# Optimization experiments

Hardware: AMD Instinct MI355X
Metric: run time of the kernel (lower is better)

The kernel has to match this reference:

```python
import jax, jax.numpy as jnp
import numpy as np

QLEN, B, D = 1024, 4, 512
H, DH = 8, 64
MEM, DMLP = 1024, 2048
KLEN = MEM + QLEN
EPS = 1e-5


def layer_norm(x, g, b):
    mu = jnp.mean(x, axis=-1, keepdims=True)
    var = jnp.var(x, axis=-1, keepdims=True)
    return (x - mu) * jax.lax.rsqrt(var + EPS) * g + b


def rel_shift(x):
    # x: [qlen, klen, b, h] -- Transformer-XL relative shift trick
    q, k, b, h = x.shape
    zp = jnp.zeros((q, 1, b, h), dtype=x.dtype)
    x = jnp.concatenate([zp, x], axis=1)          # [q, k+1, b, h]
    x = x.reshape(k + 1, q, b, h)[1:]             # drop first row
    return x.reshape(q, k, b, h)


def setup_inputs() -> dict:
    key = jax.random.key(0)
    ks = jax.random.split(key, 12)
    s = 0.02
    inp = {
        "inputs": jax.random.normal(ks[0], (QLEN, B, D), jnp.float32),
        "r": jax.random.normal(ks[1], (KLEN, D), jnp.float32),
        "u": jax.random.normal(ks[2], (H, DH), jnp.float32) * s,
        "v": jax.random.normal(ks[3], (H, DH), jnp.float32) * s,
        "mem": jax.random.normal(ks[4], (MEM, B, D), jnp.float32),
        # causal mask: query i (global pos MEM+i) cannot attend key j > MEM+i
        "attn_mask": jnp.arange(KLEN)[None, :] > (jnp.arange(QLEN)[:, None] + MEM),
        "Wqkv": jax.random.normal(ks[5], (3 * D, D), jnp.float32) * s,
        "Wr": jax.random.normal(ks[6], (D, D), jnp.float32) * s,
        "Wo": jax.random.normal(ks[7], (D, D), jnp.float32) * s,
        "ln1_g": jnp.ones((D,), jnp.float32),
        "ln1_b": jnp.zeros((D,), jnp.float32),
        "mlp_w1": jax.random.normal(ks[8], (DMLP, D), jnp.float32) * s,
        "mlp_b1": jnp.zeros((DMLP,), jnp.float32),
        "mlp_w2": jax.random.normal(ks[9], (D, DMLP), jnp.float32) * s,
        "mlp_b2": jnp.zeros((D,), jnp.float32),
        "ln2_g": jnp.ones((D,), jnp.float32),
        "ln2_b": jnp.zeros((D,), jnp.float32),
    }
    return inp


def reference(inputs, r, u, v, mem, attn_mask, Wqkv, Wr, Wo,
              ln1_g, ln1_b, mlp_w1, mlp_b1, mlp_w2, mlp_b2, ln2_g, ln2_b):
    qlen, b, d = inputs.shape
    cat = jnp.concatenate([mem, inputs], axis=0)          # [klen, b, d]
    klen = cat.shape[0]
    qkv = cat @ Wqkv.T                                    # [klen, b, 3d]
    q, k, w_v = jnp.split(qkv, 3, axis=-1)
    q = q[-qlen:].reshape(qlen, b, H, DH)
    k = k.reshape(klen, b, H, DH)
    w_v = w_v.reshape(klen, b, H, DH)
    rk = (r @ Wr.T).reshape(klen, H, DH)                  # [klen, h, dh]

    AC = jnp.einsum('ibhd,jbhd->ijbh', q + u, k)          # content term
    BD = jnp.einsum('ibhd,jhd->ijbh', q + v, rk)          # position term
    BD = rel_shift(BD)
    scale = 1.0 / np.sqrt(DH)
    score = (AC + BD) * scale                             # [q, k, b, h]
    score = jnp.where(attn_mask[:, :, None, None], jnp.float32(-1e30), score)
    prob = jax.nn.softmax(score, axis=1)
    attn = jnp.einsum('ijbh,jbhd->ibhd', prob, w_v).reshape(qlen, b, d)
    attn_out = attn @ Wo.T

    y = layer_norm(inputs + attn_out, ln1_g, ln1_b)
    h = jax.nn.relu(y @ mlp_w1.T + mlp_b1)
    z = h @ mlp_w2.T + mlp_b2
    out = layer_norm(y + z, ln2_g, ln2_b)
    return out, prob
```

## Files before the change

### kernel.cpp

```cpp
#include <hip/hip_runtime.h>
#include <math.h>

#define QL 1024
#define BSZ 4
#define DM 512
#define NH 8
#define DHH 64
#define MEML 1024
#define KL 2048
#define DMLP 2048

typedef __attribute__((ext_vector_type(8))) short bf16x8;
typedef __attribute__((ext_vector_type(4))) float f32x4;

#define MFMA16(A, B, C) __builtin_amdgcn_mfma_f32_16x16x32_bf16((A), (B), (C), 0, 0, 0)
#define SWZB(r, cb) (((r) << 7) + ((cb) ^ (((r) & 7) << 4)))
#define RINGB(r, c) (((r) << 9) + ((((c) << 2)) ^ (((r) & 7) << 4)))
#define CVT2(dst, lo, hi) \
  asm("v_cvt_pk_bf16_f32 %0, %1, %2" : "=v"(dst) : "v"(lo), "v"(hi))
#define GLOAD_LDS(gp, lp) __builtin_amdgcn_global_load_lds( \
    (const __attribute__((address_space(1))) void*)(gp), \
    (__attribute__((address_space(3))) void*)(lp), 16, 0, 0)

__device__ __forceinline__ void split_bf16(const float4 a, uint2& h, uint2& l) {
  CVT2(h.x, a.x, a.y); CVT2(h.y, a.z, a.w);
  float4 r;
  r.x = a.x - __uint_as_float(h.x << 16);
  r.y = a.y - __uint_as_float(h.x & 0xffff0000u);
  r.z = a.z - __uint_as_float(h.y << 16);
  r.w = a.w - __uint_as_float(h.y & 0xffff0000u);
  CVT2(l.x, r.x, r.y); CVT2(l.y, r.z, r.w);
}

__device__ __forceinline__ void store_tiled(char* hiB, char* loB, int KT,
                                            int row, int c0, uint2 h, uint2 l) {
  const size_t off = (((size_t)(row >> 7) * KT + (c0 >> 6)) << 14)
                   + SWZB(row & 127, (c0 & 63) * 2);
  *(uint2*)(hiB + off) = h;
  *(uint2*)(loB + off) = l;
}

__global__ __launch_bounds__(256)
void precvt_all(const float* __restrict__ mem, const float* __restrict__ inputs,
                const float* __restrict__ r, const float* __restrict__ Wqkv,
                const float* __restrict__ Wr, const float* __restrict__ Wo,
                const float* __restrict__ w1, const float* __restrict__ w2,
                unsigned short* CAThi, unsigned short* CATlo,
                unsigned short* Rhi, unsigned short* Rlo,
                unsigned short* Qhi, unsigned short* Qlo,
                unsigned short* WrHi, unsigned short* WrLo,
                unsigned short* WoHi, unsigned short* WoLo,
                unsigned short* w1Hi, unsigned short* w1Lo,
                unsigned short* w2Hi, unsigned short* w2Lo) {
  const int id = blockIdx.x * 256 + threadIdx.x;
  float4 a; uint2 h, l;
  if (id < 1048576) {
    const int row = id >> 7, c0 = (id & 127) * 4;
    const float* s = (row < 4096) ? mem + (size_t)row * 512
                                  : inputs + (size_t)(row - 4096) * 512;
    a = *(const float4*)(s + c0);
    split_bf16(a, h, l);
    store_tiled((char*)CAThi, (char*)CATlo, 8, row, c0, h, l);
  } else if (id < 1310720) {
    const int e = id - 1048576, row = e >> 7, c0 = (e & 127) * 4;
    a = *(const float4*)(r + (size_t)row * 512 + c0);
    split_bf16(a, h, l);
    store_tiled((char*)Rhi, (char*)Rlo, 8, row, c0, h, l);
  } else if (id < 1507328) {
    const int e = id - 1310720, row = e >> 7, c0 = (e & 127) * 4;
    a = *(const float4*)(Wqkv + (size_t)row * 512 + c0);
    split_bf16(a, h, l);
    store_tiled((char*)Qhi, (char*)Qlo, 8, row, c0, h, l);
  } else if (id < 1572864) {
    const int e = id - 1507328, row = e >> 7, c0 = (e & 127) * 4;
    a = *(const float4*)(Wr + (size_t)row * 512 + c0);
    split_bf16(a, h, l);
    store_tiled((char*)WrHi, (char*)WrLo, 8, row, c0, h, l);
  } else if (id < 1638400) {
    const int e = id - 1572864, row = e >> 7, c0 = (e & 127) * 4;
    a = *(const float4*)(Wo + (size_t)row * 512 + c0);
    split_bf16(a, h, l);
    store_tiled((char*)WoHi, (char*)WoLo, 8, row, c0, h, l);
  } else if (id < 1900544) {
    const int e = id - 1638400, row = e >> 7, c0 = (e & 127) * 4;
    a = *(const float4*)(w1 + (size_t)row * 512 + c0);
    split_bf16(a, h, l);
    store_tiled((char*)w1Hi, (char*)w1Lo, 8, row, c0, h, l);
  } else if (id < 2162688) {
    const int e = id - 1900544, row = e >> 9, c0 = (e & 511) * 4;
    a = *(const float4*)(w2 + (size_t)row * 2048 + c0);
    split_bf16(a, h, l);
    store_tiled((char*)w2Hi, (char*)w2Lo, 32, row, c0, h, l);
  }
}

__global__ __launch_bounds__(256)
void pack_kvr(const float* __restrict__ QKV, const float* __restrict__ RK,
              unsigned short* __restrict__ Kb, unsigned short* __restrict__ Rb,
              unsigned short* __restrict__ Vtb) {
  const int id = blockIdx.x * 256 + threadIdx.x;
  if (id < 1048576) {
    const int c4 = (id & 15) * 4;
    const int j  = (id >> 4) & 2047;
    const int bhv = id >> 15;
    const int bq = bhv >> 3, hq = bhv & 7;
    const float4 a = *(const float4*)(QKV + ((size_t)j * 4 + bq) * 1536 + 512 + hq * 64 + c4);
    uint2 p; CVT2(p.x, a.x, a.y); CVT2(p.y, a.z, a.w);
    *(uint2*)((char*)Kb + (((size_t)bhv * 32 + (j >> 6)) << 13) + SWZB(j & 63, c4 * 2)) = p;
  } else if (id < 1310720) {
    const int e = id - 1048576;
    const int c4 = (e & 15) * 4;
    const int jr = (e >> 4) & 2047;
    const int hq = e >> 15;
    const float4 a = *(const float4*)(RK + (size_t)jr * 512 + hq * 64 + c4);
    uint2 p; CVT2(p.x, a.x, a.y); CVT2(p.y, a.z, a.w);
    *(uint2*)((char*)Rb + (((size_t)hq * 32 + (jr >> 6)) << 13) + SWZB(jr & 63, c4 * 2)) = p;
  } else if (id < 1572864) {
    const int e = id - 1310720;
    const int d4 = (e & 15) * 4;
    const int jb = ((e >> 4) & 15) * 4;
    const int jt = (e >> 8) & 31;
    const int bhv = e >> 13;
    const int bq = bhv >> 3, hq = bhv & 7;
    const float* src = QKV + ((size_t)(jt * 64 + jb) * 4 + bq) * 1536 + 1024 + hq * 64 + d4;
    const float4 a0 = *(const float4*)(src);
    const float4 a1 = *(const float4*)(src + 6144);
    const float4 a2 = *(const float4*)(src + 12288);
    const float4 a3 = *(const float4*)(src + 18432);
    char* base = (char*)Vtb + (((size_t)bhv * 32 + jt) << 13);
    uint2 p;
    CVT2(p.x, a0.x, a1.x); CVT2(p.y, a2.x, a3.x);
    *(uint2*)(base + (d4 + 0) * 128 + jb * 2) = p;
    CVT2(p.x, a0.y, a1.y); CVT2(p.y, a2.y, a3.y);
    *(uint2*)(base + (d4 + 1) * 128 + jb * 2) = p;
    CVT2(p.x, a0.z, a1.z); CVT2(p.y, a2.z, a3.z);
    *(uint2*)(base + (d4 + 2) * 128 + jb * 2) = p;
    CVT2(p.x, a0.w, a1.w); CVT2(p.y, a2.w, a3.w);
    *(uint2*)(base + (d4 + 3) * 128 + jb * 2) = p;
  }
}

template<int BM, bool AGLDS, bool BIAS, bool RELU>
__global__ __launch_bounds__(256)
void gemm_nt_mfma(const float* __restrict__ A0, const float* __restrict__ A1, int M0,
                  const unsigned short* __restrict__ AhiT, const unsigned short* __restrict__ AloT,
                  const unsigned short* __restrict__ WhiT, const unsigned short* __restrict__ WloT,
                  const float* __restrict__ bias,
                  float* __restrict__ C, int M, int N, int K) {
  constexpr int MR = 4;
  constexpr int NR = (BM == 128) ? 4 : 2;
  constexpr int AU = BM / 16;
  __shared__ __align__(16) unsigned short Ahi[BM * 64];
  __shared__ __align__(16) unsigned short Alo[BM * 64];
  __shared__ __align__(16) unsigned short Bhi[128 * 64];
  __shared__ __align__(16) unsigned short Blo[128 * 64];

  const int t = threadIdx.x;
  const int w = t >> 6, lane = t & 63;
  const int lq = lane & 15, lg = lane >> 4;
  const int row0 = blockIdx.y * BM, col0 = blockIdx.x * 128;
  const int wrow0 = (BM == 128) ? (w >> 1) * 64 : 0;
  const int wcol0 = (BM == 128) ? (w & 1) * 64 : w * 32;
  const int KT = K >> 6;
  const size_t amt = (size_t)(row0 >> 7) * KT;
  const int asub = (row0 & 127) << 7;
  const size_t bnt = (size_t)(col0 >> 7) * KT;

  float4 paf[AU];
  auto loadA = [&](int k0) {
    if (!AGLDS) {
      #pragma unroll
      for (int it = 0; it < AU; ++it) {
        const int idx = it * 256 + t;
        const int row = idx >> 4, c4 = (idx & 15) * 4;
        const int grow = row0 + row;
        const float* src = (grow < M0) ? (A0 + (size_t)grow * K)
                                       : (A1 + (size_t)(grow - M0) * K);
        paf[it] = *(const float4*)(src + k0 + c4);
      }
    }
  };

  f32x4 acc[MR][NR];
  #pragma unroll
  for (int m = 0; m < MR; ++m)
    #pragma unroll
    for (int n = 0; n < NR; ++n)
      acc[m][n] = (f32x4){0.f, 0.f, 0.f, 0.f};

  loadA(0);
  for (int kt = 0; kt < KT; ++kt) {
    __syncthreads();
    {
      const char* gbh = (const char*)WhiT + ((bnt + kt) << 14);
      const char* gbl = (const char*)WloT + ((bnt + kt) << 14);
      #pragma unroll
      for (int i = 0; i < 4; ++i) {
        const int off = (w * 4 + i) * 1024;
        GLOAD_LDS(gbh + off + lane * 16, (char*)Bhi + off);
        GLOAD_LDS(gbl + off + lane * 16, (char*)Blo + off);
      }
    }
    if (AGLDS) {
      const char* gah = (const char*)AhiT + ((amt + kt) << 14) + asub;
      const char* gal = (const char*)AloT + ((amt + kt) << 14) + asub;
      #pragma unroll
      for (int i = 0; i < BM / 32; ++i) {
        const int off = (w * (BM / 32) + i) * 1024;
        GLOAD_LDS(gah + off + lane * 16, (char*)Ahi + off);
        GLOAD_LDS(gal + off + lane * 16, (char*)Alo + off);
      }
    } else {
      #pragma unroll
      for (int it = 0; it < AU; ++it) {
        const int idx = it * 256 + t;
        const int row = idx >> 4, cb = (idx & 15) * 8;
        uint2 hi, lo;
        split_bf16(paf[it], hi, lo);
        *(uint2*)((char*)Ahi + SWZB(row, cb)) = hi;
        *(uint2*)((char*)Alo + SWZB(row, cb)) = lo;
      }
    }
    __syncthreads();
    if (!AGLDS && kt + 1 < KT) loadA((kt + 1) * 64);
    #pragma unroll
    for (int ks = 0; ks < 2; ++ks) {
      bf16x8 ah[MR], al[MR], bh[NR], bl[NR];
      #pragma unroll
      for (int m = 0; m < MR; ++m) {
        ah[m] = *(const bf16x8*)((const char*)Ahi + SWZB(wrow0 + m * 16 + lq, ks * 64 + lg * 16));
        al[m] = *(const bf16x8*)((const char*)Alo + SWZB(wrow0 + m * 16 + lq, ks * 64 + lg * 16));
      }
      #pragma unroll
      for (int n = 0; n < NR; ++n) {
        bh[n] = *(const bf16x8*)((const char*)Bhi + SWZB(wcol0 + n * 16 + lq, ks * 64 + lg * 16));
        bl[n] = *(const bf16x8*)((const char*)Blo + SWZB(wcol0 + n * 16 + lq, ks * 64 + lg * 16));
      }
      #pragma unroll
      for (int m = 0; m < MR; ++m)
        #pragma unroll
        for (int n = 0; n < NR; ++n) {
          acc[m][n] = MFMA16(ah[m], bh[n], acc[m][n]);
          acc[m][n] = MFMA16(ah[m], bl[n], acc[m][n]);
          acc[m][n] = MFMA16(al[m], bh[n], acc[m][n]);
        }
    }
  }
  #pragma unroll
  for (int n = 0; n < NR; ++n) {
    const int col = col0 + wcol0 + n * 16 + lq;
    const float bv = BIAS ? bias[col] : 0.f;
    #pragma unroll
    for (int m = 0; m < MR; ++m) {
      #pragma unroll
      for (int rg = 0; rg < 4; ++rg) {
        const int row = row0 + wrow0 + m * 16 + lg * 4 + rg;
        float vv = acc[m][n][rg] + bv;
        if (RELU) vv = fmaxf(vv, 0.f);
        C[(size_t)row * N + col] = vv;
      }
    }
  }
}

__global__ __launch_bounds__(256)
void attn3_kernel(const float* __restrict__ QKV,
                  const unsigned short* __restrict__ Kb,
                  const unsigned short* __restrict__ Rb,
                  const unsigned short* __restrict__ Vtb,
                  const float* __restrict__ u, const float* __restrict__ v,
                  unsigned short* __restrict__ P, float* __restrict__ INV,
                  float* __restrict__ ATTN) {
  const int b = blockIdx.y;
  const int h = blockIdx.z;
  const int i0 = (((h >> 2) & 1) ? (15 - (int)blockIdx.x) : (int)blockIdx.x) * 64;
  const int t = threadIdx.x;
  const int w = t >> 6;
  const int lane = t & 63;
  const int lq = lane & 15;
  const int lg = lane >> 4;
  const int bh = b * 8 + h;

  __shared__ __align__(16) unsigned short Ks[2][4096];
  __shared__ __align__(16) unsigned short Rs[2][4096];
  __shared__ __align__(16) unsigned short Es[4096];
  __shared__ __align__(16) float Ring[8192];

  const int ntiles = i0 / 64 + 17;

  auto dma = [&](int jt, int jrt, int buf) {
    const char* gk = (const char*)Kb + (((size_t)bh * 32 + jt) << 13);
    const char* gr = (const char*)Rb + (((size_t)h * 32 + jrt) << 13);
    const int off = w * 2048;
    GLOAD_LDS(gk + off + lane * 16, (char*)Ks[buf] + off);
    GLOAD_LDS(gk + off + 1024 + lane * 16, (char*)Ks[buf] + off + 1024);
    GLOAD_LDS(gr + off + lane * 16, (char*)Rs[buf] + off);
    GLOAD_LDS(gr + off + 1024 + lane * 16, (char*)Rs[buf] + off + 1024);
  };

  dma(0, (1024 - i0) >> 6, 0);
  {
    const int jrtp = (960 - i0) >> 6;
    const char* gr = (const char*)Rb + (((size_t)h * 32 + jrtp) << 13);
    const int off = w * 2048;
    GLOAD_LDS(gr + off + lane * 16, (char*)Rs[1] + off);
    GLOAD_LDS(gr + off + 1024 + lane * 16, (char*)Rs[1] + off + 1024);
  }
  #pragma unroll
  for (int it = 0; it < 4; ++it) {
    const int idx = it * 256 + t;
    const int row = idx >> 4, c4 = (idx & 15) * 4;
    const float4 q4 = *(const float4*)(QKV + ((size_t)(MEML + i0 + row) * 4 + b) * 1536 + h * 64 + c4);
    const float4 u4 = *(const float4*)(u + h * 64 + c4);
    const float4 v4 = *(const float4*)(v + h * 64 + c4);
    uint2 qp;
    CVT2(qp.x, q4.x + u4.x, q4.y + u4.y); CVT2(qp.y, q4.z + u4.z, q4.w + u4.w);
    *(uint2*)((char*)Es + SWZB(row, c4 * 2)) = qp;
    CVT2(qp.x, q4.x + v4.x, q4.y + v4.y); CVT2(qp.y, q4.z + v4.z, q4.w + v4.w);
    *(uint2*)((char*)Ks[1] + SWZB(row, c4 * 2)) = qp;
  }
  __syncthreads();

  const bf16x8 qu0 = *(const bf16x8*)((const char*)Es + SWZB(w * 16 + lq, lg * 16));
  const bf16x8 qu1 = *(const bf16x8*)((const char*)Es + SWZB(w * 16 + lq, 64 + lg * 16));
  const bf16x8 qv0 = *(const bf16x8*)((const char*)Ks[1] + SWZB(w * 16 + lq, lg * 16));
  const bf16x8 qv1 = *(const bf16x8*)((const char*)Ks[1] + SWZB(w * 16 + lq, 64 + lg * 16));

  {
    f32x4 bd[4];
    #pragma unroll
    for (int nj = 0; nj < 4; ++nj) bd[nj] = (f32x4){0.f, 0.f, 0.f, 0.f};
    #pragma unroll
    for (int nj = 0; nj < 4; ++nj) {
      const bf16x8 rf0 = *(const bf16x8*)((const char*)Rs[1] + SWZB(nj * 16 + lq, lg * 16));
      const bf16x8 rf1 = *(const bf16x8*)((const char*)Rs[1] + SWZB(nj * 16 + lq, 64 + lg * 16));
      bd[nj] = MFMA16(qv0, rf0, bd[nj]);
      bd[nj] = MFMA16(qv1, rf1, bd[nj]);
    }
    #pragma unroll
    for (int nj = 0; nj < 4; ++nj) {
      const int jrl = nj * 16 + lq;
      #pragma unroll
      for (int rg = 0; rg < 4; ++rg) {
        const int il = w * 16 + lg * 4 + rg;
        *(float*)((char*)Ring + RINGB(il, 64 + jrl)) = bd[nj][rg];
      }
    }
  }

  f32x4 pv[4];
  #pragma unroll
  for (int nd = 0; nd < 4; ++nd) pv[nd] = (f32x4){0.f, 0.f, 0.f, 0.f};
  float rs[4] = {0.f, 0.f, 0.f, 0.f};

  for (int n = 0; n < ntiles; ++n) {
    const int j0 = n * 64;
    const int cur = n & 1;
    __syncthreads();
    const char* gv = (const char*)Vtb + (((size_t)bh * 32 + n) << 13);
    bf16x8 vf0[4], vf1[4];
    #pragma unroll
    for (int nd = 0; nd < 4; ++nd) {
      vf0[nd] = *(const bf16x8*)(gv + (nd * 16 + lq) * 128 + lg * 16);
      vf1[nd] = *(const bf16x8*)(gv + (nd * 16 + lq) * 128 + 64 + lg * 16);
    }
    if (n + 1 < ntiles) {
      int jrt = ((n + 1) * 64 - i0 + 1024) >> 6;
      if (jrt > 31) jrt = 31;
      dma(n + 1, jrt, cur ^ 1);
    }
    const char* KsB = (const char*)Ks[cur];
    const char* RsB = (const char*)Rs[cur];
    f32x4 acc[4], bdn[4];
    #pragma unroll
    for (int nj = 0; nj < 4; ++nj) {
      acc[nj] = (f32x4){0.f, 0.f, 0.f, 0.f};
      bdn[nj] = (f32x4){0.f, 0.f, 0.f, 0.f};
    }
    #pragma unroll
    for (int nj = 0; nj < 4; ++nj) {
      const bf16x8 kf0 = *(const bf16x8*)(KsB + SWZB(nj * 16 + lq, lg * 16));
      const bf16x8 rf0 = *(const bf16x8*)(RsB + SWZB(nj * 16 + lq, lg * 16));
      acc[nj] = MFMA16(qu0, kf0, acc[nj]);
      bdn[nj] = MFMA16(qv0, rf0, bdn[nj]);
      const bf16x8 kf1 = *(const bf16x8*)(KsB + SWZB(nj * 16 + lq, 64 + lg * 16));
      const bf16x8 rf1 = *(const bf16x8*)(RsB + SWZB(nj * 16 + lq, 64 + lg * 16));
      acc[nj] = MFMA16(qu1, kf1, acc[nj]);
      bdn[nj] = MFMA16(qv1, rf1, bdn[nj]);
    }
    const int base_cur = cur * 64;
    const int base_prev = 64 - base_cur;
    #pragma unroll
    for (int nj = 0; nj < 4; ++nj) {
      const int jrl = nj * 16 + lq;
      #pragma unroll
      for (int rg = 0; rg < 4; ++rg) {
        const int il = w * 16 + lg * 4 + rg;
        *(float*)((char*)Ring + RINGB(il, base_cur + jrl)) = bdn[nj][rg];
      }
    }
    const bool lastm = (n == ntiles - 1);
    #pragma unroll
    for (int njp = 0; njp < 2; ++njp) {
      #pragma unroll
      for (int rg = 0; rg < 4; ++rg) {
        const int il = w * 16 + lg * 4 + rg;
        float ee[2];
        #pragma unroll
        for (int q2 = 0; q2 < 2; ++q2) {
          const int nj = njp * 2 + q2;
          const int jl = nj * 16 + lq;
          const int jr_rel = jl - il + 63;
          const float ringv = (jr_rel < 64)
              ? *(const float*)((const char*)Ring + RINGB(il, base_prev + jr_rel))
              : *(const float*)((const char*)Ring + RINGB(il, base_cur + jr_rel - 64));
          const float s = 0.125f * (acc[nj][rg] + ringv);
          float e = __expf(s);
          if (lastm && jl > il) e = 0.f;
          rs[rg] += e;
          ee[q2] = e;
        }
        unsigned int pk2; CVT2(pk2, ee[0], ee[1]);
        const int jlA = (njp * 2) * 16 + lq;
        *(unsigned short*)((char*)Es + SWZB(il, jlA * 2)) = (unsigned short)(pk2 & 0xffffu);
        *(unsigned short*)((char*)Es + SWZB(il, (jlA + 16) * 2)) = (unsigned short)(pk2 >> 16);
      }
    }
    {
      const bf16x8 pf0 = *(const bf16x8*)((const char*)Es + SWZB(w * 16 + lq, lg * 16));
      const bf16x8 pf1 = *(const bf16x8*)((const char*)Es + SWZB(w * 16 + lq, 64 + lg * 16));
      #pragma unroll
      for (int nd = 0; nd < 4; ++nd) {
        pv[nd] = MFMA16(pf0, vf0[nd], pv[nd]);
        pv[nd] = MFMA16(pf1, vf1[nd], pv[nd]);
      }
    }
    #pragma unroll
    for (int it = 0; it < 2; ++it) {
      const int lin = it * 64 + lane;
      const int rr = lin >> 3, c16 = lin & 7;
      const int row = w * 16 + rr;
      const uint4 val = *(const uint4*)((const char*)Es + SWZB(row, c16 * 16));
      *(uint4*)(P + ((size_t)bh * 1024 + i0 + row) * 2048 + j0 + c16 * 8) = val;
    }
  }

  #pragma unroll
  for (int rg = 0; rg < 4; ++rg) {
    #pragma unroll
    for (int m = 1; m < 16; m <<= 1) rs[rg] += __shfl_xor(rs[rg], m, 64);
  }
  float inv[4];
  #pragma unroll
  for (int rg = 0; rg < 4; ++rg) inv[rg] = 1.0f / rs[rg];
  if (lq == 0) {
    #pragma unroll
    for (int rg = 0; rg < 4; ++rg)
      INV[(size_t)bh * 1024 + i0 + w * 16 + lg * 4 + rg] = inv[rg];
  }
  #pragma unroll
  for (int nd = 0; nd < 4; ++nd) {
    #pragma unroll
    for (int rg = 0; rg < 4; ++rg) {
      ATTN[((size_t)(i0 + w * 16 + lg * 4 + rg) * 4 + b) * 512 + h * 64 + nd * 16 + lq] =
          pv[nd][rg] * inv[rg];
    }
  }
}

__global__ __launch_bounds__(256)
void ptrans_kernel(const unsigned short* __restrict__ P, const float* __restrict__ INV,
                   float* __restrict__ prob) {
  const int i  = blockIdx.x;
  const int j0 = blockIdx.y * 64;
  const int t  = threadIdx.x;
  __shared__ float tile[32][65];
  __shared__ float invs[32];
  const bool valid = j0 <= (i & ~63) + MEML;
  if (t < 32) invs[t] = INV[(size_t)t * 1024 + i];
  if (valid) {
    const int bh = t >> 3, part = t & 7;
    const uint4 raw = *(const uint4*)(P + ((size_t)bh * 1024 + i) * 2048 + j0 + part * 8);
    const unsigned int w[4] = {raw.x, raw.y, raw.z, raw.w};
    #pragma unroll
    for (int k = 0; k < 4; ++k) {
      tile[bh][part*8 + 2*k]     = __uint_as_float(w[k] << 16);
      tile[bh][part*8 + 2*k + 1] = __uint_as_float(w[k] & 0xffff0000u);
    }
  }
  __syncthreads();
  #pragma unroll
  for (int it = 0; it < 8; ++it) {
    const int idx = it * 256 + t;
    const int jl = idx >> 5, bh = idx & 31;
    const float val = valid ? tile[bh][jl] * invs[bh] : 0.f;
    prob[((size_t)i * 2048 + j0 + jl) * 32 + bh] = val;
  }
}

__global__ __launch_bounds__(256)
void ln_res_kernel(const float* __restrict__ xa, const float* __restrict__ xb,
                   const float* __restrict__ g, const float* __restrict__ bb,
                   float* __restrict__ y) {
  const int rrow = blockIdx.x;
  const int t = threadIdx.x;
  const size_t base = (size_t)rrow * DM;
  __shared__ float red[256];
  const float a0 = xa[base + t]       + xb[base + t];
  const float a1 = xa[base + t + 256] + xb[base + t + 256];
  red[t] = a0 + a1; __syncthreads();
  for (int s = 128; s > 0; s >>= 1) { if (t < s) red[t] += red[t+s]; __syncthreads(); }
  const float mu = red[0] * (1.0f/512.0f);
  __syncthreads();
  red[t] = a0*a0 + a1*a1; __syncthreads();
  for (int s = 128; s > 0; s >>= 1) { if (t < s) red[t] += red[t+s]; __syncthreads(); }
  const float var = red[0] * (1.0f/512.0f) - mu*mu;
  const float w = rsqrtf(var + 1e-5f);
  y[base + t]       = (a0 - mu) * w * g[t]       + bb[t];
  y[base + t + 256] = (a1 - mu) * w * g[t + 256] + bb[t + 256];
}

extern "C" void kernel_launch(void* const* d_in, const int* in_sizes, int n_in,
                              void* d_out, int out_size, void* d_ws, size_t ws_size,
                              hipStream_t stream) {
  const float* inputs = (const float*)d_in[0];
  const float* r      = (const float*)d_in[1];
  const float* u      = (const float*)d_in[2];
  const float* v      = (const float*)d_in[3];
  const float* mem    = (const float*)d_in[4];
  const float* Wqkv   = (const float*)d_in[6];
  const float* Wr     = (const float*)d_in[7];
  const float* Wo     = (const float*)d_in[8];
  const float* ln1g   = (const float*)d_in[9];
  const float* ln1b   = (const float*)d_in[10];
  const float* w1     = (const float*)d_in[11];
  const float* b1     = (const float*)d_in[12];
  const float* w2     = (const float*)d_in[13];
  const float* b2     = (const float*)d_in[14];
  const float* ln2g   = (const float*)d_in[15];
  const float* ln2b   = (const float*)d_in[16];

  float* out  = (float*)d_out;
  float* prob = out + (size_t)QL*BSZ*DM;

  float* ws   = (float*)d_ws;
  unsigned short* P = (unsigned short*)ws;
  float* QKV  = ws + 33554432;
  float* RK   = QKV + 12582912;
  float* ATTN = RK + 1048576;
  float* AO   = ATTN + 2097152;
  float* Y    = AO + 2097152;
  float* INV  = Y + 2097152;
  float* HM   = ws;
  float* Z    = ws + 8388608;

  unsigned short* CAThiT = (unsigned short*)ws;
  unsigned short* CATloT = CAThiT + 4194304;
  unsigned short* RhiT   = CATloT + 4194304;
  unsigned short* RloT   = RhiT + 1048576;
  unsigned short* WqhiT  = RloT + 1048576;
  unsigned short* WqloT  = WqhiT + 786432;
  unsigned short* WrhiT  = WqloT + 786432;
  unsigned short* WrloT  = WrhiT + 262144;
  unsigned short* WohiT = (unsigned short*)(ws + 53510144);
  unsigned short* WoloT = WohiT + 262144;
  unsigned short* w1hiT = WoloT + 262144;
  unsigned short* w1loT = w1hiT + 1048576;
  unsigned short* w2hiT = w1loT + 1048576;
  unsigned short* w2loT = w2hiT + 1048576;
  unsigned short* Kb  = (unsigned short*)(ws + 55869440);
  unsigned short* Vtb = Kb + 4194304;
  unsigned short* Rb  = Vtb + 4194304;

  const dim3 blk256(256);

  precvt_all<<<dim3(8448), blk256, 0, stream>>>(
      mem, inputs, r, Wqkv, Wr, Wo, w1, w2,
      CAThiT, CATloT, RhiT, RloT, WqhiT, WqloT, WrhiT, WrloT,
      WohiT, WoloT, w1hiT, w1loT, w2hiT, w2loT);

  gemm_nt_mfma<128,true,false,false><<<dim3(12, 64), blk256, 0, stream>>>(
      nullptr, nullptr, 0, CAThiT, CATloT, WqhiT, WqloT, nullptr, QKV, 8192, 1536, 512);
  gemm_nt_mfma<64,true,false,false><<<dim3(4, 32), blk256, 0, stream>>>(
      nullptr, nullptr, 0, RhiT, RloT, WrhiT, WrloT, nullptr, RK, 2048, 512, 512);
  pack_kvr<<<dim3(6144), blk256, 0, stream>>>(QKV, RK, Kb, Rb, Vtb);
  attn3_kernel<<<dim3(16, BSZ, NH), blk256, 0, stream>>>(
      QKV, Kb, Rb, Vtb, u, v, P, INV, ATTN);
  ptrans_kernel<<<dim3(1024, 32), blk256, 0, stream>>>(P, INV, prob);

  gemm_nt_mfma<64,false,false,false><<<dim3(4, 64), blk256, 0, stream>>>(
      ATTN, ATTN, 4096, nullptr, nullptr, WohiT, WoloT, nullptr, AO, 4096, 512, 512);
  ln_res_kernel<<<dim3(4096), blk256, 0, stream>>>(inputs, AO, ln1g, ln1b, Y);
  gemm_nt_mfma<128,false,true,true><<<dim3(16, 32), blk256, 0, stream>>>(
      Y, Y, 4096, nullptr, nullptr, w1hiT, w1loT, b1, HM, 4096, 2048, 512);
  gemm_nt_mfma<64,false,true,false><<<dim3(4, 64), blk256, 0, stream>>>(
      HM, HM, 4096, nullptr, nullptr, w2hiT, w2loT, b2, Z, 4096, 512, 2048);
  ln_res_kernel<<<dim3(4096), blk256, 0, stream>>>(Y, Z, ln2g, ln2b, out);
}
```

Baseline: 660.0 us.

## Fuse bf16 packing into GEMM and producer epilogues, drop pack_kvr pass

```diff
diff --git a/kernel.cpp b/kernel.cpp
--- a/kernel.cpp
+++ b/kernel.cpp
@@ -22,14 +22,27 @@
     (const __attribute__((address_space(1))) void*)(gp), \
     (__attribute__((address_space(3))) void*)(lp), 16, 0, 0)
 
+__device__ __forceinline__ unsigned short bf16_1(float x) {
+  unsigned int t; CVT2(t, x, x); return (unsigned short)t;
+}
+__device__ __forceinline__ void split1(float x, unsigned short& h, unsigned short& l) {
+  unsigned int th; CVT2(th, x, x);
+  h = (unsigned short)th;
+  const float r = x - __uint_as_float(((unsigned int)h) << 16);
+  unsigned int tl; CVT2(tl, r, r);
+  l = (unsigned short)tl;
+}
+
 __device__ __forceinline__ void split_bf16(const float4 a, uint2& h, uint2& l) {
   CVT2(h.x, a.x, a.y); CVT2(h.y, a.z, a.w);
-  float4 r;
-  r.x = a.x - __uint_as_float(h.x << 16);
-  r.y = a.y - __uint_as_float(h.x & 0xffff0000u);
-  r.z = a.z - __uint_as_float(h.y << 16);
-  r.w = a.w - __uint_as_float(h.y & 0xffff0000u);
-  CVT2(l.x, r.x, r.y); CVT2(l.y, r.z, r.w);
+  float r;
+  float4 rr;
+  rr.x = a.x - __uint_as_float(h.x << 16);
+  rr.y = a.y - __uint_as_float(h.x & 0xffff0000u);
+  rr.z = a.z - __uint_as_float(h.y << 16);
+  rr.w = a.w - __uint_as_float(h.y & 0xffff0000u);
+  CVT2(l.x, rr.x, rr.y); CVT2(l.y, rr.z, rr.w);
+  (void)r;
 }
 
 __device__ __forceinline__ void store_tiled(char* hiB, char* loB, int KT,
@@ -94,62 +107,16 @@
   }
 }
 
+template<int BM, int EPI, bool BIAS, bool RELU>
 __global__ __launch_bounds__(256)
-void pack_kvr(const float* __restrict__ QKV, const float* __restrict__ RK,
-              unsigned short* __restrict__ Kb, unsigned short* __restrict__ Rb,
-              unsigned short* __restrict__ Vtb) {
-  const int id = blockIdx.x * 256 + threadIdx.x;
-  if (id < 1048576) {
-    const int c4 = (id & 15) * 4;
-    const int j  = (id >> 4) & 2047;
-    const int bhv = id >> 15;
-    const int bq = bhv >> 3, hq = bhv & 7;
-    const float4 a = *(const float4*)(QKV + ((size_t)j * 4 + bq) * 1536 + 512 + hq * 64 + c4);
-    uint2 p; CVT2(p.x, a.x, a.y); CVT2(p.y, a.z, a.w);
-    *(uint2*)((char*)Kb + (((size_t)bhv * 32 + (j >> 6)) << 13) + SWZB(j & 63, c4 * 2)) = p;
-  } else if (id < 1310720) {
-    const int e = id - 1048576;
-    const int c4 = (e & 15) * 4;
-    const int jr = (e >> 4) & 2047;
-    const int hq = e >> 15;
-    const float4 a = *(const float4*)(RK + (size_t)jr * 512 + hq * 64 + c4);
-    uint2 p; CVT2(p.x, a.x, a.y); CVT2(p.y, a.z, a.w);
-    *(uint2*)((char*)Rb + (((size_t)hq * 32 + (jr >> 6)) << 13) + SWZB(jr & 63, c4 * 2)) = p;
-  } else if (id < 1572864) {
-    const int e = id - 1310720;
-    const int d4 = (e & 15) * 4;
-    const int jb = ((e >> 4) & 15) * 4;
-    const int jt = (e >> 8) & 31;
-    const int bhv = e >> 13;
-    const int bq = bhv >> 3, hq = bhv & 7;
-    const float* src = QKV + ((size_t)(jt * 64 + jb) * 4 + bq) * 1536 + 1024 + hq * 64 + d4;
-    const float4 a0 = *(const float4*)(src);
-    const float4 a1 = *(const float4*)(src + 6144);
-    const float4 a2 = *(const float4*)(src + 12288);
-    const float4 a3 = *(const float4*)(src + 18432);
-    char* base = (char*)Vtb + (((size_t)bhv * 32 + jt) << 13);
-    uint2 p;
-    CVT2(p.x, a0.x, a1.x); CVT2(p.y, a2.x, a3.x);
-    *(uint2*)(base + (d4 + 0) * 128 + jb * 2) = p;
-    CVT2(p.x, a0.y, a1.y); CVT2(p.y, a2.y, a3.y);
-    *(uint2*)(base + (d4 + 1) * 128 + jb * 2) = p;
-    CVT2(p.x, a0.z, a1.z); CVT2(p.y, a2.z, a3.z);
-    *(uint2*)(base + (d4 + 2) * 128 + jb * 2) = p;
-    CVT2(p.x, a0.w, a1.w); CVT2(p.y, a2.w, a3.w);
-    *(uint2*)(base + (d4 + 3) * 128 + jb * 2) = p;
-  }
-}
-
-template<int BM, bool AGLDS, bool BIAS, bool RELU>
-__global__ __launch_bounds__(256)
-void gemm_nt_mfma(const float* __restrict__ A0, const float* __restrict__ A1, int M0,
-                  const unsigned short* __restrict__ AhiT, const unsigned short* __restrict__ AloT,
+void gemm_nt_mfma(const unsigned short* __restrict__ AhiT, const unsigned short* __restrict__ AloT,
                   const unsigned short* __restrict__ WhiT, const unsigned short* __restrict__ WloT,
                   const float* __restrict__ bias,
-                  float* __restrict__ C, int M, int N, int K) {
+                  float* __restrict__ C,
+                  unsigned short* __restrict__ X1, unsigned short* __restrict__ X2,
+                  int N, int K, int KTC) {
   constexpr int MR = 4;
   constexpr int NR = (BM == 128) ? 4 : 2;
-  constexpr int AU = BM / 16;
   __shared__ __align__(16) unsigned short Ahi[BM * 64];
   __shared__ __align__(16) unsigned short Alo[BM * 64];
   __shared__ __align__(16) unsigned short Bhi[128 * 64];
@@ -166,21 +133,6 @@
   const int asub = (row0 & 127) << 7;
   const size_t bnt = (size_t)(col0 >> 7) * KT;
 
-  float4 paf[AU];
-  auto loadA = [&](int k0) {
-    if (!AGLDS) {
-      #pragma unroll
-      for (int it = 0; it < AU; ++it) {
-        const int idx = it * 256 + t;
-        const int row = idx >> 4, c4 = (idx & 15) * 4;
-        const int grow = row0 + row;
-        const float* src = (grow < M0) ? (A0 + (size_t)grow * K)
-                                       : (A1 + (size_t)(grow - M0) * K);
-        paf[it] = *(const float4*)(src + k0 + c4);
-      }
-    }
-  };
-
   f32x4 acc[MR][NR];
   #pragma unroll
   for (int m = 0; m < MR; ++m)
@@ -188,7 +140,6 @@
     for (int n = 0; n < NR; ++n)
       acc[m][n] = (f32x4){0.f, 0.f, 0.f, 0.f};
 
-  loadA(0);
   for (int kt = 0; kt < KT; ++kt) {
     __syncthreads();
     {
@@ -201,7 +152,7 @@
         GLOAD_LDS(gbl + off + lane * 16, (char*)Blo + off);
       }
     }
-    if (AGLDS) {
+    {
       const char* gah = (const char*)AhiT + ((amt + kt) << 14) + asub;
       const char* gal = (const char*)AloT + ((amt + kt) << 14) + asub;
       #pragma unroll
@@ -210,19 +161,8 @@
         GLOAD_LDS(gah + off + lane * 16, (char*)Ahi + off);
         GLOAD_LDS(gal + off + lane * 16, (char*)Alo + off);
       }
-    } else {
-      #pragma unroll
-      for (int it = 0; it < AU; ++it) {
-        const int idx = it * 256 + t;
-        const int row = idx >> 4, cb = (idx & 15) * 8;
-        uint2 hi, lo;
-        split_bf16(paf[it], hi, lo);
-        *(uint2*)((char*)Ahi + SWZB(row, cb)) = hi;
-        *(uint2*)((char*)Alo + SWZB(row, cb)) = lo;
-      }
     }
     __syncthreads();
-    if (!AGLDS && kt + 1 < KT) loadA((kt + 1) * 64);
     #pragma unroll
     for (int ks = 0; ks < 2; ++ks) {
       bf16x8 ah[MR], al[MR], bh[NR], bl[NR];
@@ -257,20 +197,49 @@
         const int row = row0 + wrow0 + m * 16 + lg * 4 + rg;
         float vv = acc[m][n][rg] + bv;
         if (RELU) vv = fmaxf(vv, 0.f);
-        C[(size_t)row * N + col] = vv;
+        if constexpr (EPI == 0) {
+          C[(size_t)row * N + col] = vv;
+        } else if constexpr (EPI == 1) {
+          const int j = row >> 2, b = row & 3;
+          if (col0 < 512) {
+            C[(size_t)row * 512 + col] = vv;
+          } else if (col0 < 1024) {
+            const int hh = (col - 512) >> 6, d = (col - 512) & 63;
+            const size_t off = (((size_t)((b * 8 + hh) * 32 + (j >> 6))) << 13)
+                             + SWZB(j & 63, d * 2);
+            *(unsigned short*)((char*)X1 + off) = bf16_1(vv);
+          } else {
+            const int hh = (col - 1024) >> 6, d = (col - 1024) & 63;
+            const size_t off = (((size_t)((b * 8 + hh) * 32 + (j >> 6))) << 13)
+                             + d * 128 + (j & 63) * 2;
+            *(unsigned short*)((char*)X2 + off) = bf16_1(vv);
+          }
+        } else if constexpr (EPI == 2) {
+          const int hh = col >> 6, d = col & 63;
+          const size_t off = (((size_t)(hh * 32 + (row >> 6))) << 13)
+                           + SWZB(row & 63, d * 2);
+          *(unsigned short*)((char*)X1 + off) = bf16_1(vv);
+        } else {
+          unsigned short hh, ll;
+          split1(vv, hh, ll);
+          const size_t off = (((size_t)(row >> 7) * KTC + (col >> 6)) << 14)
+                           + SWZB(row & 127, (col & 63) * 2);
+          *(unsigned short*)((char*)X1 + off) = hh;
+          *(unsigned short*)((char*)X2 + off) = ll;
+        }
       }
     }
   }
 }
 
 __global__ __launch_bounds__(256)
-void attn3_kernel(const float* __restrict__ QKV,
+void attn3_kernel(const float* __restrict__ Qbuf,
                   const unsigned short* __restrict__ Kb,
                   const unsigned short* __restrict__ Rb,
                   const unsigned short* __restrict__ Vtb,
                   const float* __restrict__ u, const float* __restrict__ v,
                   unsigned short* __restrict__ P, float* __restrict__ INV,
-                  float* __restrict__ ATTN) {
+                  unsigned short* __restrict__ AThiT, unsigned short* __restrict__ ATloT) {
   const int b = blockIdx.y;
   const int h = blockIdx.z;
   const int i0 = (((h >> 2) & 1) ? (15 - (int)blockIdx.x) : (int)blockIdx.x) * 64;
@@ -310,7 +279,7 @@
   for (int it = 0; it < 4; ++it) {
     const int idx = it * 256 + t;
     const int row = idx >> 4, c4 = (idx & 15) * 4;
-    const float4 q4 = *(const float4*)(QKV + ((size_t)(MEML + i0 + row) * 4 + b) * 1536 + h * 64 + c4);
+    const float4 q4 = *(const float4*)(Qbuf + ((size_t)(MEML + i0 + row) * 4 + b) * 512 + h * 64 + c4);
     const float4 u4 = *(const float4*)(u + h * 64 + c4);
     const float4 v4 = *(const float4*)(v + h * 64 + c4);
     uint2 qp;
@@ -460,10 +429,16 @@
   }
   #pragma unroll
   for (int nd = 0; nd < 4; ++nd) {
+    const int col = h * 64 + nd * 16 + lq;
     #pragma unroll
     for (int rg = 0; rg < 4; ++rg) {
-      ATTN[((size_t)(i0 + w * 16 + lg * 4 + rg) * 4 + b) * 512 + h * 64 + nd * 16 + lq] =
-          pv[nd][rg] * inv[rg];
+      const int row = (i0 + w * 16 + lg * 4 + rg) * 4 + b;
+      unsigned short hh, ll;
+      split1(pv[nd][rg] * inv[rg], hh, ll);
+      const size_t off = (((size_t)(row >> 7) * 8 + (col >> 6)) << 14)
+                       + SWZB(row & 127, (col & 63) * 2);
+      *(unsigned short*)((char*)AThiT + off) = hh;
+      *(unsigned short*)((char*)ATloT + off) = ll;
     }
   }
 }
@@ -498,10 +473,12 @@
   }
 }
 
+template<bool SPLIT>
 __global__ __launch_bounds__(256)
 void ln_res_kernel(const float* __restrict__ xa, const float* __restrict__ xb,
                    const float* __restrict__ g, const float* __restrict__ bb,
-                   float* __restrict__ y) {
+                   float* __restrict__ y,
+                   unsigned short* __restrict__ YhiT, unsigned short* __restrict__ YloT) {
   const int rrow = blockIdx.x;
   const int t = threadIdx.x;
   const size_t base = (size_t)rrow * DM;
@@ -516,8 +493,24 @@
   for (int s = 128; s > 0; s >>= 1) { if (t < s) red[t] += red[t+s]; __syncthreads(); }
   const float var = red[0] * (1.0f/512.0f) - mu*mu;
   const float w = rsqrtf(var + 1e-5f);
-  y[base + t]       = (a0 - mu) * w * g[t]       + bb[t];
-  y[base + t + 256] = (a1 - mu) * w * g[t + 256] + bb[t + 256];
+  const float y0 = (a0 - mu) * w * g[t]       + bb[t];
+  const float y1 = (a1 - mu) * w * g[t + 256] + bb[t + 256];
+  y[base + t]       = y0;
+  y[base + t + 256] = y1;
+  if (SPLIT) {
+    unsigned short hh, ll;
+    split1(y0, hh, ll);
+    size_t off = (((size_t)(rrow >> 7) * 8 + (t >> 6)) << 14)
+               + SWZB(rrow & 127, (t & 63) * 2);
+    *(unsigned short*)((char*)YhiT + off) = hh;
+    *(unsigned short*)((char*)YloT + off) = ll;
+    split1(y1, hh, ll);
+    const int t2 = t + 256;
+    off = (((size_t)(rrow >> 7) * 8 + (t2 >> 6)) << 14)
+        + SWZB(rrow & 127, (t2 & 63) * 2);
+    *(unsigned short*)((char*)YhiT + off) = hh;
+    *(unsigned short*)((char*)YloT + off) = ll;
+  }
 }
 
 extern "C" void kernel_launch(void* const* d_in, const int* in_sizes, int n_in,
@@ -545,55 +538,60 @@
 
   float* ws   = (float*)d_ws;
   unsigned short* P = (unsigned short*)ws;
-  float* QKV  = ws + 33554432;
-  float* RK   = QKV + 12582912;
-  float* ATTN = RK + 1048576;
-  float* AO   = ATTN + 2097152;
-  float* Y    = AO + 2097152;
-  float* INV  = Y + 2097152;
-  float* HM   = ws;
-  float* Z    = ws + 8388608;
 
   unsigned short* CAThiT = (unsigned short*)ws;
   unsigned short* CATloT = CAThiT + 4194304;
-  unsigned short* RhiT   = CATloT + 4194304;
-  unsigned short* RloT   = RhiT + 1048576;
-  unsigned short* WqhiT  = RloT + 1048576;
+  unsigned short* RinhiT = CATloT + 4194304;
+  unsigned short* RinloT = RinhiT + 1048576;
+  unsigned short* WqhiT  = RinloT + 1048576;
   unsigned short* WqloT  = WqhiT + 786432;
   unsigned short* WrhiT  = WqloT + 786432;
   unsigned short* WrloT  = WrhiT + 262144;
-  unsigned short* WohiT = (unsigned short*)(ws + 53510144);
+  unsigned short* HMhiT = (unsigned short*)ws;
+  unsigned short* HMloT = HMhiT + 8388608;
+  float* Z = ws + 8388608;
+
+  float* Qbuf = ws + 33554432;
+  float* AO   = Qbuf + 4194304;
+  float* Y    = AO + 2097152;
+  float* INV  = Y + 2097152;
+  unsigned short* AThiT = (unsigned short*)(INV + 32768);
+  unsigned short* ATloT = AThiT + 2097152;
+  unsigned short* YhiT  = ATloT + 2097152;
+  unsigned short* YloT  = YhiT + 2097152;
+  unsigned short* WohiT = YloT + 2097152;
   unsigned short* WoloT = WohiT + 262144;
   unsigned short* w1hiT = WoloT + 262144;
   unsigned short* w1loT = w1hiT + 1048576;
   unsigned short* w2hiT = w1loT + 1048576;
   unsigned short* w2loT = w2hiT + 1048576;
-  unsigned short* Kb  = (unsigned short*)(ws + 55869440);
-  unsigned short* Vtb = Kb + 4194304;
-  unsigned short* Rb  = Vtb + 4194304;
+  unsigned short* Kb    = w2loT + 1048576;
+  unsigned short* Vtb   = Kb + 4194304;
+  unsigned short* Rb    = Vtb + 4194304;
 
   const dim3 blk256(256);
 
   precvt_all<<<dim3(8448), blk256, 0, stream>>>(
       mem, inputs, r, Wqkv, Wr, Wo, w1, w2,
-      CAThiT, CATloT, RhiT, RloT, WqhiT, WqloT, WrhiT, WrloT,
+      CAThiT, CATloT, RinhiT, RinloT, WqhiT, WqloT, WrhiT, WrloT,
       WohiT, WoloT, w1hiT, w1loT, w2hiT, w2loT);
 
-  gemm_nt_mfma<128,true,false,false><<<dim3(12, 64), blk256, 0, stream>>>(
-      nullptr, nullptr, 0, CAThiT, CATloT, WqhiT, WqloT, nullptr, QKV, 8192, 1536, 512);
-  gemm_nt_mfma<64,true,false,false><<<dim3(4, 32), blk256, 0, stream>>>(
-      nullptr, nullptr, 0, RhiT, RloT, WrhiT, WrloT, nullptr, RK, 2048, 512, 512);
-  pack_kvr<<<dim3(6144), blk256, 0, stream>>>(QKV, RK, Kb, Rb, Vtb);
+  gemm_nt_mfma<128,1,false,false><<<dim3(12, 64), blk256, 0, stream>>>(
+      CAThiT, CATloT, WqhiT, WqloT, nullptr, Qbuf, Kb, Vtb, 1536, 512, 0);
+  gemm_nt_mfma<64,2,false,false><<<dim3(4, 32), blk256, 0, stream>>>(
+      RinhiT, RinloT, WrhiT, WrloT, nullptr, nullptr, Rb, nullptr, 512, 512, 0);
   attn3_kernel<<<dim3(16, BSZ, NH), blk256, 0, stream>>>(
-      QKV, Kb, Rb, Vtb, u, v, P, INV, ATTN);
+      Qbuf, Kb, Rb, Vtb, u, v, P, INV, AThiT, ATloT);
   ptrans_kernel<<<dim3(1024, 32), blk256, 0, stream>>>(P, INV, prob);
 
-  gemm_nt_mfma<64,false,false,false><<<dim3(4, 64), blk256, 0, stream>>>(
-      ATTN, ATTN, 4096, nullptr, nullptr, WohiT, WoloT, nullptr, AO, 4096, 512, 512);
-  ln_res_kernel<<<dim3(4096), blk256, 0, stream>>>(inputs, AO, ln1g, ln1b, Y);
-  gemm_nt_mfma<128,false,true,true><<<dim3(16, 32), blk256, 0, stream>>>(
-      Y, Y, 4096, nullptr, nullptr, w1hiT, w1loT, b1, HM, 4096, 2048, 512);
-  gemm_nt_mfma<64,false,true,false><<<dim3(4, 64), blk256, 0, stream>>>(
-      HM, HM, 4096, nullptr, nullptr, w2hiT, w2loT, b2, Z, 4096, 512, 2048);
-  ln_res_kernel<<<dim3(4096), blk256, 0, stream>>>(Y, Z, ln2g, ln2b, out);
-}
+  gemm_nt_mfma<64,0,false,false><<<dim3(4, 64), blk256, 0, stream>>>(
+      AThiT, ATloT, WohiT, WoloT, nullptr, AO, nullptr, nullptr, 512, 512, 0);
+  ln_res_kernel<true><<<dim3(4096), blk256, 0, stream>>>(
+      inputs, AO, ln1g, ln1b, Y, YhiT, YloT);
+  gemm_nt_mfma<128,3,true,true><<<dim3(16, 32), blk256, 0, stream>>>(
+      YhiT, YloT, w1hiT, w1loT, b1, nullptr, HMhiT, HMloT, 2048, 512, 32);
+  gemm_nt_mfma<64,0,true,false><<<dim3(4, 64), blk256, 0, stream>>>(
+      HMhiT, HMloT, w2hiT, w2loT, b2, Z, nullptr, nullptr, 512, 2048, 0);
+  ln_res_kernel<false><<<dim3(4096), blk256, 0, stream>>>(
+      Y, Z, ln2g, ln2b, out, nullptr, nullptr);
+}
```

New measurement: 656.4 us. About the same (-0.5%).
